# Optimization experiments

Measured on AMD Instinct MI355X. Metric: run time of the kernel, lower is better.

Reference implementation:

```python
import jax, jax.numpy as jnp
import numpy as np

D_MODEL = 256
N_HEAD = 8


def quick_gelu(x):
    return x * jax.nn.sigmoid(1.702 * x)


def setup_inputs() -> dict:
    key = jax.random.key(0)
    ks = jax.random.split(key, 7)
    d = D_MODEL
    s = 0.02
    return {
        "x": jax.random.normal(ks[0], (2, 512, d), dtype=jnp.float32),
        "W_qkv": jax.random.normal(ks[1], (d, 3 * d), dtype=jnp.float32) * s,
        "b_qkv": jnp.zeros((3 * d,), dtype=jnp.float32),
        "W_fc": jax.random.normal(ks[2], (d, 4 * d), dtype=jnp.float32) * s,
        "b_fc": jnp.zeros((4 * d,), dtype=jnp.float32),
        "W_proj": jax.random.normal(ks[3], (4 * d, d), dtype=jnp.float32) * s,
        "b_proj": jnp.zeros((d,), dtype=jnp.float32),
    }


def attention_l1(x, W_qkv, b_qkv):
    bs, n_ctx, width = x.shape
    h = N_HEAD
    c = width // h
    scale = 1.0 / jnp.sqrt(jnp.asarray(c, x.dtype))
    qkv = (x @ W_qkv + b_qkv).reshape(bs, n_ctx, h, 3 * c)
    q, k, v = jnp.split(qkv, 3, axis=-1)  # each (b, t, h, c)
    qh = q.transpose(0, 2, 1, 3)  # (b, h, t, c)
    kh = k.transpose(0, 2, 1, 3)  # (b, h, s, c)
    vh = v.transpose(0, 2, 1, 3)  # (b, h, s, c)
    # L1 distance: sum_c |q - k| * scale  -> (b, h, t, s)
    dist = jnp.sum(jnp.abs(qh[:, :, :, None, :] - kh[:, :, None, :, :]), axis=-1) * scale
    weight = 1.0 / (0.001 + dist)
    idx = jnp.arange(n_ctx)
    weight = weight.at[:, :, idx, idx].set(0.0)
    wdtype = weight.dtype
    weight = jax.nn.softmax(weight.astype(jnp.float32), axis=-1).astype(wdtype)
    out = jnp.einsum('bhts,bhsc->bthc', weight, vh)
    return out.reshape(bs, n_ctx, width)


def reference(x, W_qkv, b_qkv, W_fc, b_fc, W_proj, b_proj):
    x = x + attention_l1(x, W_qkv, b_qkv)
    h = quick_gelu(x @ W_fc + b_fc)
    x = x + (h @ W_proj + b_proj)
    return x
```

## Files before the change

kernel.cpp:

```cpp
#include <hip/hip_runtime.h>
#include <hip/hip_bf16.h>
#include <hip/hip_fp16.h>

#define DM   256
#define NH   8
#define HC   32
#define SEQ  512
#define MTOT 1024

#define B_X1   0
#define B_QH   (1u<<20)
#define B_KH   0x180000u
#define B_VT   0x200000u
#define B_HB   0x280000u
#define B_WFCT 0x480000u
#define B_WPJT 0x500000u

typedef __attribute__((ext_vector_type(8))) __bf16 bf16x8;
typedef __attribute__((ext_vector_type(4))) __bf16 bf16x4;
typedef __attribute__((ext_vector_type(4))) float  f32x4;

__device__ __forceinline__ float qgelu(float x) {
    return x / (1.0f + __expf(-1.702f * x));
}

__global__ __launch_bounds__(256)
void qkv_k(const float* __restrict__ x, const float* __restrict__ W,
           const float* __restrict__ bias,
           const float* __restrict__ Wfc, const float* __restrict__ Wproj,
           char* __restrict__ wsb)
{
    __shared__ float lt[64 * 65];
    const int bid = blockIdx.x, tid = threadIdx.x;

    if (bid >= 768) {
        const int tt = bid - 768;
        const float* src; __bf16* dst; int K, N, tile;
        if (tt < 64) { src = Wfc;   dst = (__bf16*)(wsb + B_WFCT); K = 256;  N = 1024; tile = tt; }
        else         { src = Wproj; dst = (__bf16*)(wsb + B_WPJT); K = 1024; N = 256;  tile = tt - 64; }
        const int nn = N >> 6;
        const int k0 = (tile / nn) * 64, n0 = (tile % nn) * 64;
        const int rr0 = tid >> 4, c4 = tid & 15;
        #pragma unroll
        for (int i = 0; i < 4; ++i) {
            const int rr = rr0 + i * 16;
            float4 v = *(const float4*)&src[(size_t)(k0 + rr) * N + n0 + c4 * 4];
            lt[rr * 65 + c4 * 4 + 0] = v.x; lt[rr * 65 + c4 * 4 + 1] = v.y;
            lt[rr * 65 + c4 * 4 + 2] = v.z; lt[rr * 65 + c4 * 4 + 3] = v.w;
        }
        __syncthreads();
        #pragma unroll
        for (int i = 0; i < 4; ++i) {
            const int rr = rr0 + i * 16;
            bf16x4 b;
            b.x = (__bf16)lt[(c4 * 4 + 0) * 65 + rr];
            b.y = (__bf16)lt[(c4 * 4 + 1) * 65 + rr];
            b.z = (__bf16)lt[(c4 * 4 + 2) * 65 + rr];
            b.w = (__bf16)lt[(c4 * 4 + 3) * 65 + rr];
            *(bf16x4*)&dst[(size_t)(n0 + rr) * K + k0 + c4 * 4] = b;
        }
        return;
    }

    const int lane = tid & 63, wv = tid >> 6;
    const int widx = bid * 4 + wv;
    const int m0 = (widx & 63) * 16, n0 = (widx >> 6) * 16;
    const int r = lane & 15, q = lane >> 4;

    const float* ap = x + (size_t)(m0 + r) * DM + q * 8;
    const float* bp = W + (size_t)(q * 8) * 768 + n0 + r;

    f32x4 acc = {0.f, 0.f, 0.f, 0.f};
    #pragma unroll
    for (int kt = 0; kt < DM; kt += 32) {
        float4 a0 = *(const float4*)(ap + kt);
        float4 a1 = *(const float4*)(ap + kt + 4);
        bf16x8 af;
        af[0] = (__bf16)a0.x; af[1] = (__bf16)a0.y; af[2] = (__bf16)a0.z; af[3] = (__bf16)a0.w;
        af[4] = (__bf16)a1.x; af[5] = (__bf16)a1.y; af[6] = (__bf16)a1.z; af[7] = (__bf16)a1.w;
        bf16x8 bf;
        #pragma unroll
        for (int j = 0; j < 8; ++j)
            bf[j] = (__bf16)bp[(size_t)(kt + j) * 768];
        acc = __builtin_amdgcn_mfma_f32_16x16x32_bf16(af, bf, acc, 0, 0, 0);
    }

    __half*  qh  = (__half*)(wsb + B_QH);
    __half*  kh  = (__half*)(wsb + B_KH);
    __bf16*  vtb = (__bf16*)(wsb + B_VT);
    const int n = n0 + r;
    const float bn = bias[n];
    const int h = n / 96, jj = n % 96;
    #pragma unroll
    for (int i = 0; i < 4; ++i) {
        const int m = m0 + q * 4 + i;
        const float v = acc[i] + bn;
        const int b = m >> 9, t = m & 511;
        const int bh = b * NH + h;
        if (jj < 32)      qh[((size_t)(bh * SEQ + t)) * HC + jj]        = (__half)v;
        else if (jj < 64) kh[((size_t)(bh * SEQ + t)) * HC + (jj - 32)] = (__half)v;
        else              vtb[((size_t)(bh * HC + (jj - 64))) * SEQ + t] = (__bf16)v;
    }
}

#define QT 16
#define PSTRIDE 514

__global__ __launch_bounds__(512, 4)
void attn_k(const char* __restrict__ wsb, const float* __restrict__ xin,
            float* __restrict__ x1)
{
    __shared__ __half2 qtile[QT * 16];
    __shared__ __bf16  pmat[QT * PSTRIDE];
    __shared__ float   psum[QT * 8];
    __shared__ float   pinv[QT];

    const __half*  qhg = (const __half*)(wsb + B_QH);
    const __half*  khg = (const __half*)(wsb + B_KH);
    const __bf16*  vtb = (const __bf16*)(wsb + B_VT);

    const int tid  = threadIdx.x;
    const int lane = tid & 63;
    const int wv   = tid >> 6;
    const int sg   = tid;
    const int bh   = blockIdx.x >> 5;
    const int qbase = (blockIdx.x & 31) * QT;
    const float scale = 0.17677669529663687f;

    const __half2* kp = (const __half2*)(khg + ((size_t)(bh * SEQ + sg)) * HC);
    __half2 kr[16];
    #pragma unroll
    for (int j = 0; j < 16; ++j) kr[j] = kp[j];

    if (tid < 256) {
        const int t = tid >> 4, j = tid & 15;
        qtile[t * 16 + j] =
            *(const __half2*)(qhg + ((size_t)(bh * SEQ + qbase + t)) * HC + j * 2);
    }
    __syncthreads();

    #pragma unroll 4
    for (int t = 0; t < QT; ++t) {
        __half2 acc2 = __floats2half2_rn(0.f, 0.f);
        #pragma unroll
        for (int j = 0; j < 16; ++j) {
            __half2 dif = __hsub2(kr[j], qtile[t * 16 + j]);
            unsigned u = (*(unsigned*)&dif) & 0x7FFF7FFFu;
            acc2 = __hadd2(acc2, *(__half2*)&u);
        }
        const float d = __low2float(acc2) + __high2float(acc2);
        float w = 1.0f / (0.001f + d * scale);
        if (sg == qbase + t) w = 0.0f;
        float p = __expf(w);
        float se = p;
        #pragma unroll
        for (int off = 32; off >= 1; off >>= 1) se += __shfl_xor(se, off, 64);
        pmat[t * PSTRIDE + sg] = (__bf16)p;
        if (lane == 0) psum[t * 8 + wv] = se;
    }
    __syncthreads();

    if (tid < QT) {
        float s = 0.f;
        #pragma unroll
        for (int j = 0; j < 8; ++j) s += psum[tid * 8 + j];
        pinv[tid] = 1.0f / s;
    }
    __syncthreads();

    if (wv < 2) {
        const int r = lane & 15, q = lane >> 4;
        const __bf16* bp  = vtb + ((size_t)(bh * HC + wv * 16 + r)) * SEQ + q * 8;
        const __bf16* apm = &pmat[r * PSTRIDE + q * 8];
        f32x4 acc = {0.f, 0.f, 0.f, 0.f};
        #pragma unroll
        for (int kt = 0; kt < SEQ; kt += 32) {
            bf16x8 af = *(const bf16x8*)(apm + kt);
            bf16x8 bf = *(const bf16x8*)(bp + kt);
            acc = __builtin_amdgcn_mfma_f32_16x16x32_bf16(af, bf, acc, 0, 0, 0);
        }
        const int b = bh >> 3, hh = bh & 7;
        const int c = wv * 16 + r;
        #pragma unroll
        for (int i = 0; i < 4; ++i) {
            const int tl = q * 4 + i;
            const int t  = qbase + tl;
            const float v = acc[i] * pinv[tl];
            const int idx = ((b * SEQ + t) * DM) + hh * HC + c;
            x1[idx] = xin[idx] + v;
        }
    }
}

__global__ __launch_bounds__(256)
void fc_k(const float* __restrict__ X1, const char* __restrict__ wsb,
          const float* __restrict__ bias)
{
    const __bf16* Bt = (const __bf16*)(wsb + B_WFCT);
    __bf16* Ob = (__bf16*)(wsb + B_HB);
    const int lane = threadIdx.x & 63, wv = threadIdx.x >> 6;
    const int widx = blockIdx.x * 4 + wv;
    const int m0 = (widx & 63) * 16, n0 = (widx >> 6) * 16;
    const int r = lane & 15, q = lane >> 4;

    const float*  ap = X1 + (size_t)(m0 + r) * DM + q * 8;
    const __bf16* bp = Bt + (size_t)(n0 + r) * DM + q * 8;

    f32x4 acc = {0.f, 0.f, 0.f, 0.f};
    #pragma unroll
    for (int kt = 0; kt < DM; kt += 32) {
        float4 a0 = *(const float4*)(ap + kt);
        float4 a1 = *(const float4*)(ap + kt + 4);
        bf16x8 af;
        af[0] = (__bf16)a0.x; af[1] = (__bf16)a0.y; af[2] = (__bf16)a0.z; af[3] = (__bf16)a0.w;
        af[4] = (__bf16)a1.x; af[5] = (__bf16)a1.y; af[6] = (__bf16)a1.z; af[7] = (__bf16)a1.w;
        bf16x8 bf = *(const bf16x8*)(bp + kt);
        acc = __builtin_amdgcn_mfma_f32_16x16x32_bf16(af, bf, acc, 0, 0, 0);
    }

    const int n = n0 + r;
    const float bn = bias[n];
    #pragma unroll
    for (int i = 0; i < 4; ++i) {
        const int m = m0 + q * 4 + i;
        Ob[(size_t)m * 1024 + n] = (__bf16)qgelu(acc[i] + bn);
    }
}

__global__ __launch_bounds__(256)
void proj_k(const char* __restrict__ wsb, const float* __restrict__ bias,
            const float* __restrict__ X1, float* __restrict__ out)
{
    __shared__ f32x4 ared[4][64];
    const __bf16* H  = (const __bf16*)(wsb + B_HB);
    const __bf16* Bt = (const __bf16*)(wsb + B_WPJT);
    const int lane = threadIdx.x & 63, wv = threadIdx.x >> 6;
    const int tile = blockIdx.x;
    const int m0 = (tile & 63) * 16, n0 = (tile >> 6) * 16;
    const int r = lane & 15, q = lane >> 4;

    const __bf16* ap = H  + (size_t)(m0 + r) * 1024 + wv * 256 + q * 8;
    const __bf16* bp = Bt + (size_t)(n0 + r) * 1024 + wv * 256 + q * 8;

    f32x4 acc = {0.f, 0.f, 0.f, 0.f};
    #pragma unroll
    for (int kk = 0; kk < 8; ++kk) {
        bf16x8 af = *(const bf16x8*)(ap + kk * 32);
        bf16x8 bf = *(const bf16x8*)(bp + kk * 32);
        acc = __builtin_amdgcn_mfma_f32_16x16x32_bf16(af, bf, acc, 0, 0, 0);
    }
    ared[wv][lane] = acc;
    __syncthreads();

    if (wv == 0) {
        f32x4 a0 = ared[0][lane], a1 = ared[1][lane];
        f32x4 a2 = ared[2][lane], a3 = ared[3][lane];
        const int n = n0 + r;
        const float bn = bias[n];
        #pragma unroll
        for (int i = 0; i < 4; ++i) {
            const int m = m0 + q * 4 + i;
            const float v = a0[i] + a1[i] + a2[i] + a3[i] + bn;
            out[(size_t)m * DM + n] = X1[(size_t)m * DM + n] + v;
        }
    }
}

extern "C" void kernel_launch(void* const* d_in, const int* in_sizes, int n_in,
                              void* d_out, int out_size, void* d_ws, size_t ws_size,
                              hipStream_t stream)
{
    (void)in_sizes; (void)n_in; (void)out_size; (void)ws_size;
    const float* x     = (const float*)d_in[0];
    const float* Wqkv  = (const float*)d_in[1];
    const float* bqkv  = (const float*)d_in[2];
    const float* Wfc   = (const float*)d_in[3];
    const float* bfc   = (const float*)d_in[4];
    const float* Wproj = (const float*)d_in[5];
    const float* bproj = (const float*)d_in[6];
    float* out = (float*)d_out;
    char*  wsb = (char*)d_ws;
    float* x1  = (float*)(wsb + B_X1);

    qkv_k<<<896, 256, 0, stream>>>(x, Wqkv, bqkv, Wfc, Wproj, wsb);

    attn_k<<<512, 512, 0, stream>>>(wsb, x, x1);

    fc_k<<<1024, 256, 0, stream>>>(x1, wsb, bfc);

    proj_k<<<1024, 256, 0, stream>>>(wsb, bproj, x1, out);
}
```

Baseline: 114.5 us.

## Fuse MLP fc and proj GEMMs into one kernel with hidden tile in LDS

Replaces the separate fc and proj kernels with a single mlp_k kernel. Each block computes a 16-row slice of the quick-GELU hidden activations, keeps it in shared memory, and immediately multiplies it by the projection weights. This removes the global round trip of the bf16 hidden buffer and one kernel launch. The cost is a grid of only 64 blocks on a GPU with many CUs, so parallelism is much lower and each block does a longer serial loop.

```diff
diff --git a/kernel.cpp b/kernel.cpp
--- a/kernel.cpp
+++ b/kernel.cpp
@@ -12,9 +12,8 @@
 #define B_QH   (1u<<20)
 #define B_KH   0x180000u
 #define B_VT   0x200000u
-#define B_HB   0x280000u
-#define B_WFCT 0x480000u
-#define B_WPJT 0x500000u
+#define B_WFCT 0x280000u
+#define B_WPJT 0x300000u
 
 typedef __attribute__((ext_vector_type(8))) __bf16 bf16x8;
 typedef __attribute__((ext_vector_type(4))) __bf16 bf16x4;
@@ -192,76 +191,74 @@
     }
 }
 
-__global__ __launch_bounds__(256)
-void fc_k(const float* __restrict__ X1, const char* __restrict__ wsb,
-          const float* __restrict__ bias)
-{
-    const __bf16* Bt = (const __bf16*)(wsb + B_WFCT);
-    __bf16* Ob = (__bf16*)(wsb + B_HB);
-    const int lane = threadIdx.x & 63, wv = threadIdx.x >> 6;
-    const int widx = blockIdx.x * 4 + wv;
-    const int m0 = (widx & 63) * 16, n0 = (widx >> 6) * 16;
-    const int r = lane & 15, q = lane >> 4;
-
-    const float*  ap = X1 + (size_t)(m0 + r) * DM + q * 8;
-    const __bf16* bp = Bt + (size_t)(n0 + r) * DM + q * 8;
-
-    f32x4 acc = {0.f, 0.f, 0.f, 0.f};
-    #pragma unroll
-    for (int kt = 0; kt < DM; kt += 32) {
-        float4 a0 = *(const float4*)(ap + kt);
-        float4 a1 = *(const float4*)(ap + kt + 4);
-        bf16x8 af;
-        af[0] = (__bf16)a0.x; af[1] = (__bf16)a0.y; af[2] = (__bf16)a0.z; af[3] = (__bf16)a0.w;
-        af[4] = (__bf16)a1.x; af[5] = (__bf16)a1.y; af[6] = (__bf16)a1.z; af[7] = (__bf16)a1.w;
-        bf16x8 bf = *(const bf16x8*)(bp + kt);
-        acc = __builtin_amdgcn_mfma_f32_16x16x32_bf16(af, bf, acc, 0, 0, 0);
-    }
-
-    const int n = n0 + r;
-    const float bn = bias[n];
-    #pragma unroll
-    for (int i = 0; i < 4; ++i) {
-        const int m = m0 + q * 4 + i;
-        Ob[(size_t)m * 1024 + n] = (__bf16)qgelu(acc[i] + bn);
-    }
-}
-
-__global__ __launch_bounds__(256)
-void proj_k(const char* __restrict__ wsb, const float* __restrict__ bias,
-            const float* __restrict__ X1, float* __restrict__ out)
-{
-    __shared__ f32x4 ared[4][64];
-    const __bf16* H  = (const __bf16*)(wsb + B_HB);
-    const __bf16* Bt = (const __bf16*)(wsb + B_WPJT);
-    const int lane = threadIdx.x & 63, wv = threadIdx.x >> 6;
-    const int tile = blockIdx.x;
-    const int m0 = (tile & 63) * 16, n0 = (tile >> 6) * 16;
-    const int r = lane & 15, q = lane >> 4;
-
-    const __bf16* ap = H  + (size_t)(m0 + r) * 1024 + wv * 256 + q * 8;
-    const __bf16* bp = Bt + (size_t)(n0 + r) * 1024 + wv * 256 + q * 8;
-
-    f32x4 acc = {0.f, 0.f, 0.f, 0.f};
-    #pragma unroll
-    for (int kk = 0; kk < 8; ++kk) {
-        bf16x8 af = *(const bf16x8*)(ap + kk * 32);
-        bf16x8 bf = *(const bf16x8*)(bp + kk * 32);
-        acc = __builtin_amdgcn_mfma_f32_16x16x32_bf16(af, bf, acc, 0, 0, 0);
-    }
-    ared[wv][lane] = acc;
-    __syncthreads();
-
-    if (wv == 0) {
-        f32x4 a0 = ared[0][lane], a1 = ared[1][lane];
-        f32x4 a2 = ared[2][lane], a3 = ared[3][lane];
-        const int n = n0 + r;
-        const float bn = bias[n];
-        #pragma unroll
-        for (int i = 0; i < 4; ++i) {
-            const int m = m0 + q * 4 + i;
-            const float v = a0[i] + a1[i] + a2[i] + a3[i] + bn;
-            out[(size_t)m * DM + n] = X1[(size_t)m * DM + n] + v;
+#define HSTR 1032
+
+__global__ __launch_bounds__(512)
+void mlp_k(const float* __restrict__ X1, const char* __restrict__ wsb,
+           const float* __restrict__ bfc, const float* __restrict__ bproj,
+           float* __restrict__ out)
+{
+    __shared__ __bf16 hl[16 * HSTR];
+    const __bf16* Wf = (const __bf16*)(wsb + B_WFCT);
+    const __bf16* Wp = (const __bf16*)(wsb + B_WPJT);
+
+    const int tid  = threadIdx.x;
+    const int lane = tid & 63;
+    const int wv   = tid >> 6;
+    const int m0   = blockIdx.x * 16;
+    const int r    = lane & 15, q = lane >> 4;
+
+    {
+        const float* ap = X1 + (size_t)(m0 + r) * DM + q * 8;
+        f32x4 acc[8] = {};
+        #pragma unroll
+        for (int kt = 0; kt < DM; kt += 32) {
+            float4 a0 = *(const float4*)(ap + kt);
+            float4 a1 = *(const float4*)(ap + kt + 4);
+            bf16x8 af;
+            af[0] = (__bf16)a0.x; af[1] = (__bf16)a0.y; af[2] = (__bf16)a0.z; af[3] = (__bf16)a0.w;
+            af[4] = (__bf16)a1.x; af[5] = (__bf16)a1.y; af[6] = (__bf16)a1.z; af[7] = (__bf16)a1.w;
+            #pragma unroll
+            for (int nt = 0; nt < 8; ++nt) {
+                const int n0 = (wv * 8 + nt) * 16;
+                bf16x8 bf = *(const bf16x8*)(Wf + (size_t)(n0 + r) * DM + q * 8 + kt);
+                acc[nt] = __builtin_amdgcn_mfma_f32_16x16x32_bf16(af, bf, acc[nt], 0, 0, 0);
+            }
+        }
+        #pragma unroll
+        for (int nt = 0; nt < 8; ++nt) {
+            const int n = (wv * 8 + nt) * 16 + r;
+            const float bn = bfc[n];
+            #pragma unroll
+            for (int i = 0; i < 4; ++i)
+                hl[(q * 4 + i) * HSTR + n] = (__bf16)qgelu(acc[nt][i] + bn);
+        }
+    }
+    __syncthreads();
+
+    {
+        f32x4 acc[2] = {};
+        const __bf16* al = &hl[r * HSTR + q * 8];
+        #pragma unroll 4
+        for (int kt = 0; kt < 1024; kt += 32) {
+            bf16x8 af = *(const bf16x8*)(al + kt);
+            #pragma unroll
+            for (int nt = 0; nt < 2; ++nt) {
+                const int n0 = (wv * 2 + nt) * 16;
+                bf16x8 bf = *(const bf16x8*)(Wp + (size_t)(n0 + r) * 1024 + q * 8 + kt);
+                acc[nt] = __builtin_amdgcn_mfma_f32_16x16x32_bf16(af, bf, acc[nt], 0, 0, 0);
+            }
+        }
+        #pragma unroll
+        for (int nt = 0; nt < 2; ++nt) {
+            const int n = (wv * 2 + nt) * 16 + r;
+            const float bn = bproj[n];
+            #pragma unroll
+            for (int i = 0; i < 4; ++i) {
+                const int m = m0 + q * 4 + i;
+                out[(size_t)m * DM + n] =
+                    X1[(size_t)m * DM + n] + acc[nt][i] + bn;
+            }
         }
     }
 }
@@ -286,7 +283,5 @@
 
     attn_k<<<512, 512, 0, stream>>>(wsb, x, x1);
 
-    fc_k<<<1024, 256, 0, stream>>>(x1, wsb, bfc);
-
-    proj_k<<<1024, 256, 0, stream>>>(wsb, bproj, x1, out);
-}
+    mlp_k<<<64, 512, 0, stream>>>(x1, wsb, bfc, bproj, out);
+}
```

Measured after the change: 126.8 us. 1.11x slower.
